# Optimization experiments

Hardware: AMD Instinct MI355X
Metric: run time of the kernel (lower is better)

## Reference

```python
import jax, jax.numpy as jnp
import numpy as np

B, T, D, H, E, O, A = 8192, 223, 7, 128, 50, 29, 9
IMPUTE_W, LABEL_W = 0.3, 1.0

def setup_inputs() -> dict:
    key = jax.random.key(0)
    ks = jax.random.split(key, 32)
    u = lambda k, shape, fan: jax.random.uniform(k, shape, jnp.float32, -1.0/np.sqrt(fan), 1.0/np.sqrt(fan))
    return {
        'values':    jax.random.normal(ks[0], (B, T, D), jnp.float32),
        'masks':     (jax.random.uniform(ks[1], (B, T, D)) < 0.8).astype(jnp.float32),
        'deltas':    jax.random.uniform(ks[2], (B, T, D), jnp.float32) * 5.0,
        'probs':     jax.nn.softmax(jax.random.normal(ks[3], (B, O), jnp.float32), axis=1),
        'ancillary': jax.random.normal(ks[4], (B, A), jnp.float32),
        'labels':    jax.random.randint(ks[5], (B,), 0, O, jnp.int32),
        'W_td_h': u(ks[6], (H, D), H),  'b_td_h': u(ks[7], (H,), H),
        'W_td_x': u(ks[8], (D, D), D),  'b_td_x': u(ks[9], (D,), D),
        'W_hist': u(ks[10], (D, H), H), 'b_hist': u(ks[11], (D,), H),
        'W_feat': u(ks[12], (D, D), D), 'b_feat': u(ks[13], (D,), D),
        'W_comb': u(ks[14], (D, 2*D), 2*D), 'b_comb': u(ks[15], (D,), 2*D),
        'W_ih': u(ks[16], (4*H, 2*D), H), 'W_hh': u(ks[17], (4*H, H), H),
        'b_ih': u(ks[18], (4*H,), H),     'b_hh': u(ks[19], (4*H,), H),
        'W_anc': u(ks[20], (E, A), A),    'b_anc': u(ks[21], (E,), A),
        'W_cat': u(ks[22], (H, H + E), H + E), 'b_cat': u(ks[23], (H,), H + E),
        'W_out': u(ks[24], (O, H), H),    'b_out': u(ks[25], (O,), H),
    }

def _rits_forward(values, masks, deltas, probs, ancillary,
                  W_td_h, b_td_h, W_td_x, b_td_x, W_hist, b_hist,
                  W_feat, b_feat, W_comb, b_comb, W_ih, W_hh, b_ih, b_hh,
                  W_anc, b_anc, W_cat, b_cat, W_out, b_out):
    Bn = values.shape[0]
    td_x_diag = jnp.diag(W_td_x)                     # diag=True decay uses only diagonal
    Wf = W_feat * (1.0 - jnp.eye(D, dtype=W_feat.dtype))

    def step(carry, xt):
        h, c, xl = carry
        x, m, d = xt                                  # each [B, D]
        gamma_h = jnp.exp(-jax.nn.relu(d @ W_td_h.T + b_td_h))   # [B, H]
        gamma_x = jnp.exp(-jax.nn.relu(d * td_x_diag + b_td_x))  # [B, D]
        h = h * gamma_h
        x_h = h @ W_hist.T + b_hist
        msum = jnp.sum(m) + 1e-5
        xl = xl + jnp.sum(jnp.abs(x - x_h) * m) / msum
        x_c = m * x + (1.0 - m) * x_h
        z_h = x_c @ Wf.T + b_feat
        xl = xl + jnp.sum(jnp.abs(x - z_h) * m) / msum
        alpha = jnp.concatenate([gamma_x, m], axis=1) @ W_comb.T + b_comb
        c_h = alpha * z_h + (1.0 - alpha) * x_h
        xl = xl + jnp.sum(jnp.abs(x - c_h) * m) / msum
        c_c = m * x + (1.0 - m) * c_h
        inputs = jnp.concatenate([c_c, m], axis=1)    # [B, 2D]
        gates = inputs @ W_ih.T + b_ih + h @ W_hh.T + b_hh  # [B, 4H]
        i, f, g, o = jnp.split(gates, 4, axis=1)
        c = jax.nn.sigmoid(f) * c + jax.nn.sigmoid(i) * jnp.tanh(g)
        h = jax.nn.sigmoid(o) * jnp.tanh(c)
        return (h, c, xl), c_c

    h0 = jnp.zeros((Bn, H), values.dtype)
    c0 = jnp.zeros((Bn, H), values.dtype)
    xs = (jnp.swapaxes(values, 0, 1), jnp.swapaxes(masks, 0, 1), jnp.swapaxes(deltas, 0, 1))
    (h, c, x_loss), imps = jax.lax.scan(step, (h0, c0, jnp.float32(0.0)), xs)
    imputations = jnp.swapaxes(imps, 0, 1)           # [B, T, D]

    x_loss = x_loss * IMPUTE_W
    anc = jax.nn.relu(ancillary @ W_anc.T + b_anc)
    h = jax.nn.relu(jnp.concatenate([h, anc], axis=1) @ W_cat.T + b_cat)
    y_h = jax.nn.softmax(h @ W_out.T + b_out, axis=1)
    y_loss = jnp.sum((y_h - probs) ** 2) / (Bn + 1e-5) * LABEL_W
    return x_loss, y_loss, x_loss + y_loss, y_h, imputations

def reference(values, masks, deltas, probs, ancillary, labels,
              W_td_h, b_td_h, W_td_x, b_td_x, W_hist, b_hist,
              W_feat, b_feat, W_comb, b_comb, W_ih, W_hh, b_ih, b_hh,
              W_anc, b_anc, W_cat, b_cat, W_out, b_out):
    x_loss, y_loss, loss, y_h, imputations = _rits_forward(
        values, masks, deltas, probs, ancillary,
        W_td_h, b_td_h, W_td_x, b_td_x, W_hist, b_hist,
        W_feat, b_feat, W_comb, b_comb, W_ih, W_hh, b_ih, b_hh,
        W_anc, b_anc, W_cat, b_cat, W_out, b_out)
    return (x_loss, y_loss, loss, y_h, imputations, labels)
```

## Files before the change

kernel.cpp:

```cpp
#include <hip/hip_runtime.h>
#include <math.h>

#define B_ 8192
#define T_ 223
#define D_ 7
#define H_ 128
#define E_ 50
#define O_ 29
#define A_ 9
#define TD_ (T_*D_)
#define NB 32
#define NTHR 512
#define MB 8
#define MS_BG 128

#define WS_MINV  0
#define WS_ACC   (WS_MINV + T_)
#define WS_WCATT (WS_ACC + 2)
#define WS_HFIN  (WS_WCATT + 178*H_)

#define OUT_YH  3
#define OUT_IMP (OUT_YH + B_*O_)
#define OUT_LAB (OUT_IMP + B_*T_*D_)

typedef __attribute__((ext_vector_type(8))) short short8;
typedef __attribute__((ext_vector_type(4))) float floatx4;
#define MFMA16(Av,Bv,Cv) __builtin_amdgcn_mfma_f32_16x16x32_bf16((Av),(Bv),(Cv),0,0,0)

#define BARRIER() do { asm volatile("s_waitcnt lgkmcnt(0)" ::: "memory"); \
                       __builtin_amdgcn_s_barrier(); } while (0)

__device__ __forceinline__ unsigned short f2bf(float f) {
    unsigned int u = __builtin_bit_cast(unsigned int, f);
    return (unsigned short)((u + 0x7FFFu + ((u >> 16) & 1u)) >> 16);
}
__device__ __forceinline__ float bf2f(unsigned short s) {
    unsigned int u = ((unsigned int)s) << 16;
    return __builtin_bit_cast(float, u);
}
__device__ __forceinline__ float rcp_(float x)  { return __builtin_amdgcn_rcpf(x); }
__device__ __forceinline__ float sigm(float x)  { return rcp_(1.f + __expf(-x)); }
__device__ __forceinline__ float tanh_(float x) { return 1.f - 2.f*rcp_(1.f + __expf(2.f*x)); }

__global__ void rits_prep(const float* __restrict__ W_cat, float* __restrict__ ws)
{
    int idx = blockIdx.x * 256 + threadIdx.x;
    if (idx < H_*178) {
        int j = idx / 178, k = idx - j*178;
        ws[WS_WCATT + k*H_ + j] = W_cat[idx];
    }
    if (idx < T_) ws[WS_MINV + idx] = 0.f;
    if (idx < 2) ws[WS_ACC + idx] = 0.f;
}

__global__ void rits_msum(const float* __restrict__ masks, float* __restrict__ ws)
{
    const int tc = blockIdx.x % 7;
    const int bg = blockIdx.x / 7;
    const int t0 = tc * 32;
    const int nt = (t0 + 32 <= T_) ? 32 : (T_ - t0);
    const int ncol = nt * D_;
    const int tid = threadIdx.x;
    __shared__ float sums[224];
    float s = 0.f;
    if (tid < ncol) {
        const int bpg = B_ / MS_BG;
        const float* p = masks + (size_t)bg * bpg * TD_ + (size_t)t0 * D_ + tid;
        #pragma unroll 4
        for (int b = 0; b < bpg; ++b) s += p[(size_t)b * TD_];
    }
    if (tid < 224) sums[tid] = (tid < ncol) ? s : 0.f;
    __syncthreads();
    if (tid < 32) {
        float r = 0.f;
        #pragma unroll
        for (int q = 0; q < 7; ++q) r += sums[tid*7 + q];
        if (t0 + tid < T_) atomicAdd(&ws[WS_MINV + t0 + tid], r);
    }
}

__global__ __launch_bounds__(NTHR, 2) void rits_main(
    const float* __restrict__ values, const float* __restrict__ masks, const float* __restrict__ deltas,
    const float* __restrict__ W_td_h, const float* __restrict__ b_td_h,
    const float* __restrict__ W_td_x, const float* __restrict__ b_td_x,
    const float* __restrict__ W_hist, const float* __restrict__ b_hist,
    const float* __restrict__ W_feat, const float* __restrict__ b_feat,
    const float* __restrict__ W_comb, const float* __restrict__ b_comb,
    const float* __restrict__ W_ih, const float* __restrict__ W_hh,
    const float* __restrict__ b_ih, const float* __restrict__ b_hh,
    float* __restrict__ ws, float* __restrict__ out)
{
    __shared__ __attribute__((aligned(16))) unsigned short hbuf[NB*168];
    __shared__ __attribute__((aligned(16))) unsigned short bbuf[NB*32];
    __shared__ __attribute__((aligned(16))) unsigned short whis_lds[16*136];
    __shared__ float xm_l[NB*18];
    __shared__ float gx_l[NB*9];
    __shared__ float xh_l[NB*10];
    __shared__ float impbuf[NB*16*7];
    __shared__ float red[8];

    const int tid  = threadIdx.x;
    const int b0   = blockIdx.x * NB;
    const int lane = tid & 63;
    const int w    = tid >> 6;
    const int quad = lane >> 4;
    const int l15  = lane & 15;

    for (int i = tid; i < NB*168; i += NTHR) hbuf[i] = 0;
    for (int i = tid; i < NB*32;  i += NTHR) bbuf[i] = 0;
    for (int i = tid; i < 16*136; i += NTHR) {
        int r = i / 136, c = i - r*136;
        whis_lds[i] = (r < 7 && c < 128) ? f2bf(W_hist[r*H_ + c]) : 0;
    }
    __syncthreads();
    if (tid < NB) {
        bbuf[tid*32 + 7]  = 0x3F80;
        bbuf[tid*32 + 15] = 0x3F80;
    }

    short8 whhf[4][4];
    short8 winf_c[4];
    short8 winf_mb[4];
    short8 wtdf;
    float  bh_r[4];
    {
        union UU { short8 v; unsigned short u[8]; } fr;
        #pragma unroll
        for (int c = 0; c < 4; ++c) {
            const int j = (c*8 + w)*16 + l15;
            #pragma unroll
            for (int s = 0; s < 4; ++s) {
                const float* p = W_hh + j*H_ + s*32 + quad*8;
                #pragma unroll
                for (int e = 0; e < 8; ++e) fr.u[e] = f2bf(p[e]);
                whhf[c][s] = fr.v;
            }
            #pragma unroll
            for (int e = 0; e < 8; ++e) {
                int k = quad*8 + e;
                fr.u[e] = (k < 7) ? f2bf(W_ih[j*14 + k]) : (unsigned short)0;
            }
            winf_c[c] = fr.v;
            #pragma unroll
            for (int e = 0; e < 8; ++e) {
                int k = quad*8 + e;
                float v = (k < 7) ? W_ih[j*14 + 7 + k]
                        : ((k == 7) ? (b_ih[j] + b_hh[j]) : 0.f);
                fr.u[e] = f2bf(v);
            }
            winf_mb[c] = fr.v;
        }
        const int j2 = w*16 + l15;
        #pragma unroll
        for (int e = 0; e < 8; ++e) {
            int k = quad*8 + e;
            float v = (k >= 8 && k < 15) ? W_td_h[j2*D_ + (k - 8)]
                    : ((k == 15) ? b_td_h[j2] : 0.f);
            fr.u[e] = f2bf(v);
        }
        wtdf = fr.v;
        #pragma unroll
        for (int r = 0; r < 4; ++r) {
            int f = quad*4 + r;
            bh_r[r] = (quad < 2 && f < 7) ? b_hist[f] : 0.f;
        }
    }

    const bool ldr = (tid < NB*D_);
    const int  lb  = tid / D_, li = tid - (tid/D_)*D_;
    float wfr[7], wcr[14], bfr = 0.f, bcr = 0.f, tdx_own = 0.f, btdx_own = 0.f;
    if (ldr) {
        #pragma unroll
        for (int k = 0; k < 7; ++k)  wfr[k] = (k == li) ? 0.f : W_feat[li*D_ + k];
        #pragma unroll
        for (int k = 0; k < 14; ++k) wcr[k] = W_comb[li*14 + k];
        bfr = b_feat[li];  bcr = b_comb[li];
        tdx_own = W_td_x[li*D_ + li];  btdx_own = b_td_x[li];
    }

    float c_st[2][4] = {{0,0,0,0},{0,0,0,0}};
    float lacc = 0.f;

    const long gbase = (long)(b0 + lb)*TD_ + li;
    float rx = 0.f, rm = 0.f, rd = 0.f;
    const float* msums = ws + WS_MINV;
    float rmv = 0.f;
    if (ldr) { rx = values[gbase]; rm = masks[gbase]; rd = deltas[gbase]; rmv = msums[0]; }

    for (int t = 0; t < T_; ++t) {
        if (ldr) {
            float2 s2 = { rx, rm };
            *(float2*)&xm_l[lb*18 + 2*li] = s2;
            gx_l[lb*9 + li] = __expf(-fmaxf(fmaf(rd, tdx_own, btdx_own), 0.f));
            bbuf[lb*32 + li] = f2bf(rm);
            if (t + 1 < T_) {
                const long g = gbase + (long)(t+1)*D_;
                rx = values[g]; rm = masks[g]; rd = deltas[g];
                rmv = msums[t+1] ;
            }
        }
        const float invt = rcp_((ldr ? (t ? rmv : msums[t]) : 0.f) + 1e-5f);
        BARRIER();

        floatx4 acc[4][2];
        #pragma unroll
        for (int c = 0; c < 4; ++c)
            #pragma unroll
            for (int nt = 0; nt < 2; ++nt) { floatx4 z = {0,0,0,0}; acc[c][nt] = z; }
        floatx4 xh0 = {0,0,0,0}, xh1 = {0,0,0,0};
        #pragma unroll
        for (int s = 0; s < 4; ++s) {
            short8 hb0 = *(const short8*)&hbuf[l15*168       + s*32 + quad*8];
            short8 hb1 = *(const short8*)&hbuf[(16+l15)*168  + s*32 + quad*8];
            #pragma unroll
            for (int c = 0; c < 4; ++c) {
                acc[c][0] = MFMA16(whhf[c][s], hb0, acc[c][0]);
                acc[c][1] = MFMA16(whhf[c][s], hb1, acc[c][1]);
            }
            if (w == 7) {
                short8 wh = *(const short8*)&whis_lds[l15*136 + s*32 + quad*8];
                xh0 = MFMA16(wh, hb0, xh0);
                xh1 = MFMA16(wh, hb1, xh1);
            }
        }
        if (w == 7 && quad < 2) {
            #pragma unroll
            for (int nt = 0; nt < 2; ++nt) {
                const int b = nt*16 + l15;
                floatx4 xv = nt ? xh1 : xh0;
                float2 p0 = { xv[0] + bh_r[0], xv[1] + bh_r[1] };
                float2 p1 = { xv[2] + bh_r[2], xv[3] + bh_r[3] };
                *(float2*)&xh_l[b*10 + quad*4]     = p0;
                *(float2*)&xh_l[b*10 + quad*4 + 2] = p1;
            }
        }
        BARRIER();

        {
            short8 bb0 = *(const short8*)&bbuf[l15*32      + quad*8];
            short8 bb1 = *(const short8*)&bbuf[(16+l15)*32 + quad*8];
            #pragma unroll
            for (int c = 0; c < 4; ++c) {
                acc[c][0] = MFMA16(winf_mb[c], bb0, acc[c][0]);
                acc[c][1] = MFMA16(winf_mb[c], bb1, acc[c][1]);
            }
        }

        if (ldr) {
            const int b = lb, i = li;
            const float x = xm_l[b*18 + 2*i], m = xm_l[b*18 + 2*i + 1];
            const float xhv = xh_l[b*10 + i];
            float zh = bfr, al = bcr;
            #pragma unroll
            for (int k = 0; k < 7; ++k) {
                const float xk  = xm_l[b*18 + 2*k];
                const float mk  = xm_l[b*18 + 2*k + 1];
                const float xhk = xh_l[b*10 + k];
                const float xck = mk*xk + (1.f - mk)*xhk;
                zh = fmaf(wfr[k], xck, zh);
                al = fmaf(wcr[k], gx_l[b*9 + k], al);
                al = fmaf(wcr[7+k], mk, al);
            }
            const float ch = al*zh + (1.f - al)*xhv;
            const float cc = m*x + (1.f - m)*ch;
            impbuf[(b*16 + (t & 15))*7 + i] = cc;
            hbuf[b*168 + 128 + i] = f2bf(cc);
            lacc = fmaf((fabsf(x-xhv) + fabsf(x-zh) + fabsf(x-ch)) * m, invt, lacc);
            if (t + 1 < T_)
                bbuf[lb*32 + 8 + li] = f2bf(rd);
        }
        BARRIER();

        {
            short8 ib0 = *(const short8*)&hbuf[l15*168      + 128 + quad*8];
            short8 ib1 = *(const short8*)&hbuf[(16+l15)*168 + 128 + quad*8];
            #pragma unroll
            for (int c = 0; c < 4; ++c) {
                acc[c][0] = MFMA16(winf_c[c], ib0, acc[c][0]);
                acc[c][1] = MFMA16(winf_c[c], ib1, acc[c][1]);
            }
        }
        const bool dec = (t + 1 < T_);
        floatx4 g0 = {0,0,0,0}, g1 = {0,0,0,0};
        if (dec) {
            short8 bb0 = *(const short8*)&bbuf[l15*32      + quad*8];
            short8 bb1 = *(const short8*)&bbuf[(16+l15)*32 + quad*8];
            floatx4 z = {0,0,0,0};
            g0 = MFMA16(wtdf, bb0, z);
            g1 = MFMA16(wtdf, bb1, z);
        }
        #pragma unroll
        for (int nt = 0; nt < 2; ++nt) {
            const int b = nt*16 + l15;
            floatx4 gg = nt ? g1 : g0;
            float hnv[4];
            #pragma unroll
            for (int r = 0; r < 4; ++r) {
                float ig = acc[0][nt][r], fg = acc[1][nt][r];
                float gv = acc[2][nt][r], og = acc[3][nt][r];
                float cn = sigm(fg)*c_st[nt][r] + sigm(ig)*tanh_(gv);
                c_st[nt][r] = cn;
                float hn = sigm(og)*tanh_(cn);
                if (dec) hn *= __expf(-fmaxf(gg[r], 0.f));
                hnv[r] = hn;
            }
            uint2 pk;
            pk.x = (unsigned)f2bf(hnv[0]) | ((unsigned)f2bf(hnv[1]) << 16);
            pk.y = (unsigned)f2bf(hnv[2]) | ((unsigned)f2bf(hnv[3]) << 16);
            *(uint2*)&hbuf[b*168 + w*16 + quad*4] = pk;
        }

        if ((t & 15) == 15 || t == T_ - 1) {
            const int t0 = t & ~15;
            const int b  = tid >> 4, c16 = tid & 15;
            if (t0 + c16 <= t) {
                float* gp = out + (size_t)OUT_IMP + (size_t)(b0+b)*TD_ + (size_t)(t0+c16)*D_;
                const float* lp = &impbuf[(b*16 + c16)*7];
                #pragma unroll
                for (int e = 0; e < 7; ++e) gp[e] = lp[e];
            }
        }
    }
    __syncthreads();

    for (int off = 32; off > 0; off >>= 1) lacc += __shfl_down(lacc, off, 64);
    if ((tid & 63) == 0) red[tid >> 6] = lacc;
    __syncthreads();
    if (tid == 0) {
        float s = 0.f;
        #pragma unroll
        for (int q = 0; q < 8; ++q) s += red[q];
        atomicAdd(&ws[WS_ACC], s);
    }
    for (int i = tid; i < NB*H_; i += NTHR) {
        int b = i >> 7, j = i & 127;
        ws[WS_HFIN + (size_t)(b0+b)*H_ + j] = bf2f(hbuf[b*168 + j]);
    }
}

__global__ __launch_bounds__(128) void rits_head(
    const float* __restrict__ probs, const float* __restrict__ ancillary, const int* __restrict__ labels,
    const float* __restrict__ W_anc, const float* __restrict__ b_anc,
    const float* __restrict__ b_cat,
    const float* __restrict__ W_out, const float* __restrict__ b_out,
    float* __restrict__ ws, float* __restrict__ out)
{
    __shared__ float hb[MB*H_];
    __shared__ float ancl[MB*52];
    __shared__ float hc[MB*H_];
    __shared__ float lg[MB*32];
    __shared__ float smx[MB], sinv[MB], ysum[MB];
    __shared__ float sq[MB*32];
    const int tid = threadIdx.x;
    const int bb0 = blockIdx.x * MB;

    for (int i = tid; i < MB*H_; i += 128) hb[i] = ws[WS_HFIN + (size_t)bb0*H_ + i];
    for (int i = tid; i < MB*E_; i += 128) {
        int b = i / E_, e = i - b*E_;
        float s = b_anc[e];
        #pragma unroll
        for (int a = 0; a < A_; ++a) s = fmaf(ancillary[(bb0+b)*A_ + a], W_anc[e*A_ + a], s);
        ancl[b*52+e] = fmaxf(s, 0.f);
    }
    __syncthreads();
    {
        const int j = tid;
        float s[MB];
        #pragma unroll
        for (int b = 0; b < MB; ++b) s[b] = b_cat[j];
        const float* wc = ws + WS_WCATT;
        for (int k = 0; k < H_; ++k) {
            float wv = wc[k*H_ + j];
            #pragma unroll
            for (int b = 0; b < MB; ++b) s[b] = fmaf(hb[b*H_+k], wv, s[b]);
        }
        for (int k = 0; k < E_; ++k) {
            float wv = wc[(H_+k)*H_ + j];
            #pragma unroll
            for (int b = 0; b < MB; ++b) s[b] = fmaf(ancl[b*52+k], wv, s[b]);
        }
        #pragma unroll
        for (int b = 0; b < MB; ++b) hc[b*H_+j] = fmaxf(s[b], 0.f);
    }
    __syncthreads();
    for (int i = tid; i < MB*O_; i += 128) {
        int b = i / O_, o = i - b*O_;
        float s = b_out[o];
        for (int k = 0; k < H_; ++k) s = fmaf(hc[b*H_+k], W_out[o*H_+k], s);
        lg[b*32+o] = s;
    }
    __syncthreads();
    if (tid < MB) {
        float mx = -1e30f;
        for (int o = 0; o < O_; ++o) mx = fmaxf(mx, lg[tid*32+o]);
        float se = 0.f;
        for (int o = 0; o < O_; ++o) se += __expf(lg[tid*32+o] - mx);
        smx[tid] = mx; sinv[tid] = 1.f / se;
    }
    __syncthreads();
    for (int i = tid; i < MB*O_; i += 128) {
        int b = i / O_, o = i - b*O_;
        float y = __expf(lg[b*32+o] - smx[b]) * sinv[b];
        out[OUT_YH + (size_t)(bb0+b)*O_ + o] = y;
        float d = y - probs[(size_t)(bb0+b)*O_ + o];
        sq[b*32+o] = d*d;
    }
    __syncthreads();
    if (tid < MB) {
        float s = 0.f;
        for (int o = 0; o < O_; ++o) s += sq[tid*32+o];
        ysum[tid] = s;
        out[OUT_LAB + bb0 + tid] = (float)labels[bb0 + tid];
    }
    __syncthreads();
    if (tid == 0) {
        float s = 0.f;
        #pragma unroll
        for (int b = 0; b < MB; ++b) s += ysum[b];
        atomicAdd(&ws[WS_ACC+1], s);
    }
}

__global__ void rits_fin(const float* __restrict__ ws, float* __restrict__ out)
{
    if (blockIdx.x == 0 && threadIdx.x == 0) {
        float xl = ws[WS_ACC] * 0.3f;
        float yl = ws[WS_ACC+1] * (1.0f / (8192.0f + 1e-5f));
        out[0] = xl; out[1] = yl; out[2] = xl + yl;
    }
}

extern "C" void kernel_launch(void* const* d_in, const int* in_sizes, int n_in,
                              void* d_out, int out_size, void* d_ws, size_t ws_size,
                              hipStream_t stream)
{
    const float* values = (const float*)d_in[0];
    const float* masks  = (const float*)d_in[1];
    const float* deltas = (const float*)d_in[2];
    const float* probs  = (const float*)d_in[3];
    const float* ancil  = (const float*)d_in[4];
    const int*   labels = (const int*)  d_in[5];
    const float* W_td_h = (const float*)d_in[6];
    const float* b_td_h = (const float*)d_in[7];
    const float* W_td_x = (const float*)d_in[8];
    const float* b_td_x = (const float*)d_in[9];
    const float* W_hist = (const float*)d_in[10];
    const float* b_hist = (const float*)d_in[11];
    const float* W_feat = (const float*)d_in[12];
    const float* b_feat = (const float*)d_in[13];
    const float* W_comb = (const float*)d_in[14];
    const float* b_comb = (const float*)d_in[15];
    const float* W_ih   = (const float*)d_in[16];
    const float* W_hh   = (const float*)d_in[17];
    const float* b_ih   = (const float*)d_in[18];
    const float* b_hh   = (const float*)d_in[19];
    const float* W_anc  = (const float*)d_in[20];
    const float* b_anc  = (const float*)d_in[21];
    const float* W_cat  = (const float*)d_in[22];
    const float* b_cat  = (const float*)d_in[23];
    const float* W_out  = (const float*)d_in[24];
    const float* b_out  = (const float*)d_in[25];
    float* ws  = (float*)d_ws;
    float* out = (float*)d_out;

    hipLaunchKernelGGL(rits_prep, dim3((H_*178 + 255)/256), dim3(256), 0, stream, W_cat, ws);
    hipLaunchKernelGGL(rits_msum, dim3(7*MS_BG), dim3(256), 0, stream, masks, ws);
    hipLaunchKernelGGL(rits_main, dim3(B_/NB), dim3(NTHR), 0, stream,
                       values, masks, deltas, W_td_h, b_td_h, W_td_x, b_td_x,
                       W_hist, b_hist, W_feat, b_feat, W_comb, b_comb,
                       W_ih, W_hh, b_ih, b_hh, ws, out);
    hipLaunchKernelGGL(rits_head, dim3(B_/MB), dim3(128), 0, stream,
                       probs, ancil, labels, W_anc, b_anc, b_cat, W_out, b_out, ws, out);
    hipLaunchKernelGGL(rits_fin, dim3(1), dim3(1), 0, stream, ws, out);
}
```

Before: 875.3 us.

## Halve per-block batch to 16 rows to double block count

Reduces the number of batch rows handled per workgroup from 32 to 16, so each wave runs one MFMA N-tile instead of two and the grid doubles to 512 blocks. The sequential recurrence over time is latency-bound, so spreading the batch across more blocks should fill more compute units on the 256-CU device. In exchange, each block does half the MFMA work per barrier, so barrier and LDS overhead make up a larger share of each step. The imputation write-back is guarded to the smaller row count.

```diff
diff --git a/kernel.cpp b/kernel.cpp
--- a/kernel.cpp
+++ b/kernel.cpp
@@ -9,7 +9,7 @@
 #define O_ 29
 #define A_ 9
 #define TD_ (T_*D_)
-#define NB 32
+#define NB 16
 #define NTHR 512
 #define MB 8
 #define MS_BG 128
@@ -178,7 +178,7 @@
         tdx_own = W_td_x[li*D_ + li];  btdx_own = b_td_x[li];
     }
 
-    float c_st[2][4] = {{0,0,0,0},{0,0,0,0}};
+    float c_st[4] = {0,0,0,0};
     float lacc = 0.f;
 
     const long gbase = (long)(b0 + lb)*TD_ + li;
@@ -188,6 +188,7 @@
     if (ldr) { rx = values[gbase]; rm = masks[gbase]; rd = deltas[gbase]; rmv = msums[0]; }
 
     for (int t = 0; t < T_; ++t) {
+        float msum_cur = rmv;
         if (ldr) {
             float2 s2 = { rx, rm };
             *(float2*)&xm_l[lb*18 + 2*li] = s2;
@@ -196,58 +197,45 @@
             if (t + 1 < T_) {
                 const long g = gbase + (long)(t+1)*D_;
                 rx = values[g]; rm = masks[g]; rd = deltas[g];
-                rmv = msums[t+1] ;
-            }
-        }
-        const float invt = rcp_((ldr ? (t ? rmv : msums[t]) : 0.f) + 1e-5f);
+                rmv = msums[t+1];
+            }
+        }
         BARRIER();
 
-        floatx4 acc[4][2];
-        #pragma unroll
-        for (int c = 0; c < 4; ++c)
-            #pragma unroll
-            for (int nt = 0; nt < 2; ++nt) { floatx4 z = {0,0,0,0}; acc[c][nt] = z; }
-        floatx4 xh0 = {0,0,0,0}, xh1 = {0,0,0,0};
+        floatx4 acc[4];
+        #pragma unroll
+        for (int c = 0; c < 4; ++c) { floatx4 z = {0,0,0,0}; acc[c] = z; }
+        floatx4 xh0 = {0,0,0,0};
         #pragma unroll
         for (int s = 0; s < 4; ++s) {
-            short8 hb0 = *(const short8*)&hbuf[l15*168       + s*32 + quad*8];
-            short8 hb1 = *(const short8*)&hbuf[(16+l15)*168  + s*32 + quad*8];
-            #pragma unroll
-            for (int c = 0; c < 4; ++c) {
-                acc[c][0] = MFMA16(whhf[c][s], hb0, acc[c][0]);
-                acc[c][1] = MFMA16(whhf[c][s], hb1, acc[c][1]);
-            }
+            short8 hb0 = *(const short8*)&hbuf[l15*168 + s*32 + quad*8];
+            #pragma unroll
+            for (int c = 0; c < 4; ++c)
+                acc[c] = MFMA16(whhf[c][s], hb0, acc[c]);
             if (w == 7) {
                 short8 wh = *(const short8*)&whis_lds[l15*136 + s*32 + quad*8];
                 xh0 = MFMA16(wh, hb0, xh0);
-                xh1 = MFMA16(wh, hb1, xh1);
             }
         }
         if (w == 7 && quad < 2) {
-            #pragma unroll
-            for (int nt = 0; nt < 2; ++nt) {
-                const int b = nt*16 + l15;
-                floatx4 xv = nt ? xh1 : xh0;
-                float2 p0 = { xv[0] + bh_r[0], xv[1] + bh_r[1] };
-                float2 p1 = { xv[2] + bh_r[2], xv[3] + bh_r[3] };
-                *(float2*)&xh_l[b*10 + quad*4]     = p0;
-                *(float2*)&xh_l[b*10 + quad*4 + 2] = p1;
-            }
+            const int b = l15;
+            float2 p0 = { xh0[0] + bh_r[0], xh0[1] + bh_r[1] };
+            float2 p1 = { xh0[2] + bh_r[2], xh0[3] + bh_r[3] };
+            *(float2*)&xh_l[b*10 + quad*4]     = p0;
+            *(float2*)&xh_l[b*10 + quad*4 + 2] = p1;
         }
         BARRIER();
 
         {
-            short8 bb0 = *(const short8*)&bbuf[l15*32      + quad*8];
-            short8 bb1 = *(const short8*)&bbuf[(16+l15)*32 + quad*8];
-            #pragma unroll
-            for (int c = 0; c < 4; ++c) {
-                acc[c][0] = MFMA16(winf_mb[c], bb0, acc[c][0]);
-                acc[c][1] = MFMA16(winf_mb[c], bb1, acc[c][1]);
-            }
+            short8 bb0 = *(const short8*)&bbuf[l15*32 + quad*8];
+            #pragma unroll
+            for (int c = 0; c < 4; ++c)
+                acc[c] = MFMA16(winf_mb[c], bb0, acc[c]);
         }
 
         if (ldr) {
             const int b = lb, i = li;
+            const float invt = rcp_(msum_cur + 1e-5f);
             const float x = xm_l[b*18 + 2*i], m = xm_l[b*18 + 2*i + 1];
             const float xhv = xh_l[b*10 + i];
             float zh = bfr, al = bcr;
@@ -272,36 +260,29 @@
         BARRIER();
 
         {
-            short8 ib0 = *(const short8*)&hbuf[l15*168      + 128 + quad*8];
-            short8 ib1 = *(const short8*)&hbuf[(16+l15)*168 + 128 + quad*8];
-            #pragma unroll
-            for (int c = 0; c < 4; ++c) {
-                acc[c][0] = MFMA16(winf_c[c], ib0, acc[c][0]);
-                acc[c][1] = MFMA16(winf_c[c], ib1, acc[c][1]);
-            }
+            short8 ib0 = *(const short8*)&hbuf[l15*168 + 128 + quad*8];
+            #pragma unroll
+            for (int c = 0; c < 4; ++c)
+                acc[c] = MFMA16(winf_c[c], ib0, acc[c]);
         }
         const bool dec = (t + 1 < T_);
-        floatx4 g0 = {0,0,0,0}, g1 = {0,0,0,0};
+        floatx4 g0 = {0,0,0,0};
         if (dec) {
-            short8 bb0 = *(const short8*)&bbuf[l15*32      + quad*8];
-            short8 bb1 = *(const short8*)&bbuf[(16+l15)*32 + quad*8];
+            short8 bb0 = *(const short8*)&bbuf[l15*32 + quad*8];
             floatx4 z = {0,0,0,0};
             g0 = MFMA16(wtdf, bb0, z);
-            g1 = MFMA16(wtdf, bb1, z);
-        }
-        #pragma unroll
-        for (int nt = 0; nt < 2; ++nt) {
-            const int b = nt*16 + l15;
-            floatx4 gg = nt ? g1 : g0;
+        }
+        {
+            const int b = l15;
             float hnv[4];
             #pragma unroll
             for (int r = 0; r < 4; ++r) {
-                float ig = acc[0][nt][r], fg = acc[1][nt][r];
-                float gv = acc[2][nt][r], og = acc[3][nt][r];
-                float cn = sigm(fg)*c_st[nt][r] + sigm(ig)*tanh_(gv);
-                c_st[nt][r] = cn;
+                float ig = acc[0][r], fg = acc[1][r];
+                float gv = acc[2][r], og = acc[3][r];
+                float cn = sigm(fg)*c_st[r] + sigm(ig)*tanh_(gv);
+                c_st[r] = cn;
                 float hn = sigm(og)*tanh_(cn);
-                if (dec) hn *= __expf(-fmaxf(gg[r], 0.f));
+                if (dec) hn *= __expf(-fmaxf(g0[r], 0.f));
                 hnv[r] = hn;
             }
             uint2 pk;
@@ -313,7 +294,7 @@
         if ((t & 15) == 15 || t == T_ - 1) {
             const int t0 = t & ~15;
             const int b  = tid >> 4, c16 = tid & 15;
-            if (t0 + c16 <= t) {
+            if (b < NB && t0 + c16 <= t) {
                 float* gp = out + (size_t)OUT_IMP + (size_t)(b0+b)*TD_ + (size_t)(t0+c16)*D_;
                 const float* lp = &impbuf[(b*16 + c16)*7];
                 #pragma unroll
```

Measured after the change: 1.028 ms. +17.5%, slower.
